# Performance work log

Hardware: AMD Instinct MI355X
Metric: run time of the kernel (lower is better)

Reference implementation:

```python
import jax, jax.numpy as jnp
import numpy as np

B, S, T = 4096, 32, 32   # batch (flattened words), source chars, target chars
V = 256                  # char vocab (source and target)
E, H, A = 128, 64, 64    # source embed, GRU units, attention dim
BOW = 1                  # begin-of-word token id


def setup_inputs() -> dict:
    key = jax.random.key(0)
    ks = iter(jax.random.split(key, 32))
    p = lambda shape: jax.random.normal(next(ks), shape, dtype=jnp.float32) * 0.05
    return {
        "src_ids": jax.random.randint(next(ks), (B, S), 0, V, dtype=jnp.int64),
        "tgt_ids": jax.random.randint(next(ks), (B, T), 0, V, dtype=jnp.int64),
        "src_emb": p((V, E)),
        "enc_Wf": p((E, 3 * H)), "enc_Uf": p((H, 3 * H)), "enc_bf": p((2, 3 * H)),
        "enc_Wb": p((E, 3 * H)), "enc_Ub": p((H, 3 * H)), "enc_bb": p((2, 3 * H)),
        "attn_We": p((H, A)), "attn_be": p((A,)),
        "attn_Wd": p((H, A)), "attn_bd": p((A,)),
        "attn_v": p((A, 1)), "attn_bv": p((1,)),
        "dec_W": p((H + H, 3 * H)), "dec_U": p((H, 3 * H)), "dec_b": p((2, 3 * H)),
        "out_W": p((H, V)), "out_b": p((V,)),
    }


def _gru_cell(h, x, W, U, b):
    # TF GRUCell with reset_after=True (default): separate input/recurrent biases
    xp = x @ W + b[0]
    hp = h @ U + b[1]
    xz, xr, xh = jnp.split(xp, 3, axis=-1)
    hz, hr, hh = jnp.split(hp, 3, axis=-1)
    z = jax.nn.sigmoid(xz + hz)
    r = jax.nn.sigmoid(xr + hr)
    n = jnp.tanh(xh + r * hh)
    return z * h + (1.0 - z) * n


def _gru_scan(xs, h0, W, U, b):
    # xs: [S, B, D] -> outputs [S, B, H]
    def step(h, x):
        h_new = _gru_cell(h, x, W, U, b)
        return h_new, h_new
    _, ys = jax.lax.scan(step, h0, xs)
    return ys


def reference(src_ids, tgt_ids, src_emb,
              enc_Wf, enc_Uf, enc_bf, enc_Wb, enc_Ub, enc_bb,
              attn_We, attn_be, attn_Wd, attn_bd, attn_v, attn_bv,
              dec_W, dec_U, dec_b, out_W, out_b):
    batch = src_ids.shape[0]
    # --- encoder: embedding + bidirectional GRU (merge_mode='sum') ---
    emb = src_emb[src_ids]                       # [B,S,E]
    xs = jnp.swapaxes(emb, 0, 1)                 # [S,B,E]
    h0 = jnp.zeros((batch, H), emb.dtype)
    fwd = _gru_scan(xs, h0, enc_Wf, enc_Uf, enc_bf)
    bwd = _gru_scan(xs[::-1], h0, enc_Wb, enc_Ub, enc_bb)[::-1]
    encoded = jnp.swapaxes(fwd + bwd, 0, 1)      # [B,S,H]

    # --- attention memory setup ---
    enc_proj = encoded @ attn_We + attn_be       # [B,S,A]

    # --- decoder inputs: BOW-prefixed teacher-forced targets, tied embedding ---
    dec_in = jnp.concatenate(
        [jnp.full((batch, 1), BOW, dtype=tgt_ids.dtype), tgt_ids[:, :-1]], axis=1)
    tied_table = out_W.T * jnp.sqrt(jnp.asarray(H, encoded.dtype))  # [V,H]
    dec_emb = tied_table[dec_in]                 # [B,T,H]

    # --- decoder: Bahdanau-attention GRU, scan over time ---
    def step(h, x):
        dproj = h @ attn_Wd + attn_bd                        # [B,A]
        s = jnp.tanh(dproj[:, None, :] + enc_proj)           # [B,S,A]
        logit = (s @ attn_v)[..., 0] + attn_bv[0]            # [B,S]
        w = jax.nn.softmax(logit, axis=1)                    # softmax over S
        ctx = jnp.einsum('bs,bsh->bh', w, encoded)           # [B,H]
        att_in = jnp.concatenate([x, ctx], axis=1)           # [B,2H]
        h_new = _gru_cell(h, att_in, dec_W, dec_U, dec_b)
        return h_new, h_new

    _, hs = jax.lax.scan(step, encoded[:, 0], jnp.swapaxes(dec_emb, 0, 1))
    hidden = jnp.swapaxes(hs, 0, 1)              # [B,T,H]
    logits = hidden @ out_W + out_b              # [B,T,V]
    return logits
```

## Files before the change

### kernel.cpp

```cpp
#include <hip/hip_runtime.h>
#include <hip/hip_bf16.h>

typedef unsigned short u16;
typedef __bf16  bf16x8 __attribute__((ext_vector_type(8)));
typedef float   f32x4  __attribute__((ext_vector_type(4)));
typedef unsigned int   u32x4 __attribute__((ext_vector_type(4)));
typedef unsigned short u16x4 __attribute__((ext_vector_type(4)));

union FragU { bf16x8 v; u16 u[8]; u32x4 q; };

__device__ __forceinline__ float b2f(u16 u) {
    unsigned int x = ((unsigned int)u) << 16;
    return __builtin_bit_cast(float, x);
}
__device__ __forceinline__ u16 f2b(float f) {
    unsigned int x = __builtin_bit_cast(unsigned int, f);
    unsigned int r = (x + 0x7fffu + ((x >> 16) & 1u)) >> 16;
    return (u16)r;
}
__device__ __forceinline__ float rcp_(float x) { return __builtin_amdgcn_rcpf(x); }
__device__ __forceinline__ float sigm_(float x) { return rcp_(1.0f + __expf(-x)); }
__device__ __forceinline__ float tanh_(float x) {
    float e = __expf(2.0f * x);
    return 1.0f - 2.0f * rcp_(e + 1.0f);
}
__device__ __forceinline__ bf16x8 load_afrag(const u16* s) {
    FragU f; f.q = *(const u32x4*)s; return f.v;
}
__device__ __forceinline__ f32x4 mfma16(bf16x8 a, bf16x8 b, f32x4 c) {
    return __builtin_amdgcn_mfma_f32_16x16x32_bf16(a, b, c, 0, 0, 0);
}
__device__ __forceinline__ void split2(float f, u16& hi, u16& lo) {
    hi = f2b(f); lo = f2b(f - b2f(hi));
}

template<int MODE, int K, int N>
__device__ __forceinline__ void gemm_body(
    const float* __restrict__ srcf, const u16* __restrict__ sh,
    const u16* __restrict__ sl, const u16* __restrict__ sh2,
    const u16* __restrict__ sl2, const float* __restrict__ W,
    const float* __restrict__ bias, float* __restrict__ outf,
    u16* __restrict__ outh, int rbase)
{
    constexpr int KP = K + 8;
    constexpr int LK = (K == 128) ? 7 : 6;
    __shared__ __attribute__((aligned(16))) u16 Ash[64 * KP];
    __shared__ __attribute__((aligned(16))) u16 Asl[64 * KP];

    const int tid  = threadIdx.x;
    const int lane = tid & 63, w = tid >> 6;
    const int q = lane >> 4, ln = lane & 15;

    for (int i = tid; i < 64 * K; i += 256) {
        int r = i >> LK, c = i & (K - 1);
        int rg = rbase + r;
        float f;
        if constexpr (MODE == 0)      f = srcf[rg * K + c];
        else if constexpr (MODE == 1) f = srcf[c * 256 + rg] * 8.0f;
        else if constexpr (MODE == 2)
            f = b2f(sh[rg * 64 + c]) + b2f(sl[rg * 64 + c])
              + b2f(sh2[rg * 64 + c]) + b2f(sl2[rg * 64 + c]);
        else                          f = b2f(sh[rg * 64 + c]) + b2f(sl[rg * 64 + c]);
        u16 hi, lo; split2(f, hi, lo);
        Ash[r * KP + c] = hi; Asl[r * KP + c] = lo;
    }

    constexpr int NT  = N / 64;
    constexpr int NKF = K / 32;
    FragU bfh[NT][NKF], bfl[NT][NKF];
    float bv[NT];
    const int cw = w * (N >> 2);
#pragma unroll
    for (int tl = 0; tl < NT; ++tl) {
        int col = cw + tl * 16 + ln;
#pragma unroll
        for (int kf = 0; kf < NKF; ++kf)
#pragma unroll
            for (int j = 0; j < 8; ++j) {
                float f = W[(kf * 32 + q * 8 + j) * N + col];
                split2(f, bfh[tl][kf].u[j], bfl[tl][kf].u[j]);
            }
        bv[tl] = bias[col];
    }
    __syncthreads();

#pragma unroll
    for (int r = 0; r < 4; ++r) {
        bf16x8 afh[NKF], afl[NKF];
#pragma unroll
        for (int kf = 0; kf < NKF; ++kf) {
            afh[kf] = load_afrag(&Ash[(r * 16 + ln) * KP + kf * 32 + q * 8]);
            afl[kf] = load_afrag(&Asl[(r * 16 + ln) * KP + kf * 32 + q * 8]);
        }
#pragma unroll
        for (int tl = 0; tl < NT; ++tl) {
            f32x4 acc = {0.f, 0.f, 0.f, 0.f};
#pragma unroll
            for (int kf = 0; kf < NKF; ++kf) {
                acc = mfma16(afl[kf], bfh[tl][kf].v, acc);
                acc = mfma16(afh[kf], bfl[tl][kf].v, acc);
                acc = mfma16(afh[kf], bfh[tl][kf].v, acc);
            }
            const int col = cw + tl * 16 + ln;
#pragma unroll
            for (int i = 0; i < 4; ++i) {
                int rowg = rbase + r * 16 + q * 4 + i;
                float val = acc[i] + bv[tl];
                if constexpr (MODE == 2) {
                    outh[rowg * 64 + col] = f2b(val * 2.0f);
                } else if constexpr (MODE == 3) {
                    outf[rowg * N + col] = val;
                } else {
                    outf[rowg * 192 + col] = val;
                }
            }
        }
    }
}

template<int MODE, int K, int N>
__global__ __launch_bounds__(256, (MODE >= 2) ? 2 : 1) void gemm_hl(
    const float* __restrict__ srcf, const u16* __restrict__ sh,
    const u16* __restrict__ sl, const u16* __restrict__ sh2,
    const u16* __restrict__ sl2, const float* __restrict__ W,
    const float* __restrict__ bias, float* __restrict__ outf,
    u16* __restrict__ outh)
{
    gemm_body<MODE, K, N>(srcf, sh, sl, sh2, sl2, W, bias, outf, outh,
                          (int)blockIdx.x * 64);
}

__global__ __launch_bounds__(256, 1) void xpv_all(
    const float* __restrict__ src_emb,
    const float* __restrict__ Wf, const float* __restrict__ bf, float* __restrict__ xf,
    const float* __restrict__ Wb, const float* __restrict__ bb, float* __restrict__ xb,
    const float* __restrict__ outW, const float* __restrict__ dW,
    const float* __restrict__ db, float* __restrict__ xd)
{
    const int b = blockIdx.x;
    if (b < 4)
        gemm_body<0, 128, 192>(src_emb, nullptr, nullptr, nullptr, nullptr,
                               Wf, bf, xf, nullptr, b * 64);
    else if (b < 8)
        gemm_body<0, 128, 192>(src_emb, nullptr, nullptr, nullptr, nullptr,
                               Wb, bb, xb, nullptr, (b - 4) * 64);
    else
        gemm_body<1, 64, 192>(outW, nullptr, nullptr, nullptr, nullptr,
                              dW, db, xd, nullptr, (b - 8) * 64);
}

__global__ __launch_bounds__(256, 2) void enc8(
    const int* __restrict__ src_ids, const float* __restrict__ xf,
    const float* __restrict__ xb,
    const float* __restrict__ Uf_, const float* __restrict__ bf_,
    const float* __restrict__ Ub_, const float* __restrict__ bb_,
    u16* __restrict__ fh, u16* __restrict__ fl,
    u16* __restrict__ bh, u16* __restrict__ bl)
{
    __shared__ __attribute__((aligned(16))) u16 hsh[16 * 72];
    __shared__ __attribute__((aligned(16))) u16 hsl[16 * 72];
    const int tid  = threadIdx.x;
    const int lane = tid & 63, w = tid >> 6;
    const int q = lane >> 4, ln = lane & 15;
    const int dir = (int)(blockIdx.x >> 9);
    const int b0  = (int)(blockIdx.x & 511) * 8;
    const float* xpv = dir ? xb  : xf;
    const float* U   = dir ? Ub_ : Uf_;
    const float* b_  = dir ? bb_ : bf_;
    u16* oh = dir ? bh : fh;
    u16* ol = dir ? bl : fl;
    const int jw = w * 16;
    const bool rowok = (q < 2);

    for (int i = tid; i < 16 * 64; i += 256) {
        int r = i >> 6, c = i & 63;
        hsh[r * 72 + c] = 0; hsl[r * 72 + c] = 0;
    }
    FragU ufh[3][2], ufl[3][2];
    float b1[3];
#pragma unroll
    for (int g = 0; g < 3; ++g) {
        int col = g * 64 + jw + ln;
#pragma unroll
        for (int kf = 0; kf < 2; ++kf)
#pragma unroll
            for (int j = 0; j < 8; ++j) {
                float f = U[(kf * 32 + q * 8 + j) * 192 + col];
                split2(f, ufh[g][kf].u[j], ufl[g][kf].u[j]);
            }
        b1[g] = b_[192 + col];
    }
    float hp[4] = {0, 0, 0, 0};

    float xg[3][4];
    {
        const int s0 = dir ? 31 : 0;
#pragma unroll
        for (int i = 0; i < 4; ++i) {
            int rowv = b0 + ((q * 4 + i) & 7);
            int id = src_ids[rowv * 32 + s0];
#pragma unroll
            for (int g = 0; g < 3; ++g) xg[g][i] = xpv[id * 192 + g * 64 + jw + ln];
        }
    }
    __syncthreads();

    for (int step = 0; step < 32; ++step) {
        const int s = dir ? (31 - step) : step;
        float xgn[3][4];
        {
            int sn = dir ? (step >= 31 ? 0 : 30 - step) : (step >= 31 ? 31 : step + 1);
#pragma unroll
            for (int i = 0; i < 4; ++i) {
                int rowv = b0 + ((q * 4 + i) & 7);
                int id = src_ids[rowv * 32 + sn];
#pragma unroll
                for (int g = 0; g < 3; ++g) xgn[g][i] = xpv[id * 192 + g * 64 + jw + ln];
            }
        }
        bf16x8 a0h = load_afrag(&hsh[ln * 72 + q * 8]);
        bf16x8 a1h = load_afrag(&hsh[ln * 72 + 32 + q * 8]);
        bf16x8 a0l = load_afrag(&hsl[ln * 72 + q * 8]);
        bf16x8 a1l = load_afrag(&hsl[ln * 72 + 32 + q * 8]);
        f32x4 acc[3];
#pragma unroll
        for (int g = 0; g < 3; ++g) {
            f32x4 a = {0.f, 0.f, 0.f, 0.f};
            a = mfma16(a0l, ufh[g][0].v, a);
            a = mfma16(a0h, ufl[g][0].v, a);
            a = mfma16(a0h, ufh[g][0].v, a);
            a = mfma16(a1l, ufh[g][1].v, a);
            a = mfma16(a1h, ufl[g][1].v, a);
            a = mfma16(a1h, ufh[g][1].v, a);
            acc[g] = a;
        }
        float nh[4];
#pragma unroll
        for (int i = 0; i < 4; ++i) {
            const int rowg = b0 + q * 4 + i;
            float zz = sigm_(xg[0][i] + acc[0][i] + b1[0]);
            float rr = sigm_(xg[1][i] + acc[1][i] + b1[1]);
            float nn = tanh_(xg[2][i] + rr * (acc[2][i] + b1[2]));
            nh[i] = zz * hp[i] + (1.0f - zz) * nn;  hp[i] = nh[i];
            if (rowok) {
                const int gidx = (rowg * 32 + s) * 64 + jw + ln;
                u16 hi, lo; split2(nh[i], hi, lo);
                oh[gidx] = hi; ol[gidx] = lo;
            }
        }
        __syncthreads();
        if (rowok) {
#pragma unroll
            for (int i = 0; i < 4; ++i) {
                u16 hi, lo; split2(nh[i], hi, lo);
                hsh[(q * 4 + i) * 72 + jw + ln] = hi;
                hsl[(q * 4 + i) * 72 + jw + ln] = lo;
            }
        }
        __syncthreads();
#pragma unroll
        for (int g = 0; g < 3; ++g)
#pragma unroll
            for (int i = 0; i < 4; ++i) xg[g][i] = xgn[g][i];
    }
}

__global__ __launch_bounds__(256, 2) void dec_kernel(
    const int* __restrict__ tgt_ids, const float* __restrict__ xpvd,
    const u16* __restrict__ fh, const u16* __restrict__ fl,
    const u16* __restrict__ bh, const u16* __restrict__ bl,
    const u16* __restrict__ encpT,
    const float* __restrict__ dec_U, const float* __restrict__ dec_W,
    const float* __restrict__ dec_b,
    const float* __restrict__ Wd, const float* __restrict__ bd,
    const float* __restrict__ v_, const float* __restrict__ bv_,
    u16* __restrict__ hid_hi, u16* __restrict__ hid_lo)
{
    __shared__ __attribute__((aligned(16))) float enc_lds[8 * 2048];
    __shared__ __attribute__((aligned(16))) u16 hqh[16 * 72];
    __shared__ __attribute__((aligned(16))) u16 hql[16 * 72];
    __shared__ __attribute__((aligned(16))) u16 cxh[16 * 72];
    __shared__ __attribute__((aligned(16))) u16 cxl[16 * 72];
    __shared__ __attribute__((aligned(16))) float dpl[8 * 72];
    __shared__ float wl[8 * 36];
    __shared__ float vl[64];
    const int tid  = threadIdx.x;
    const int lane = tid & 63, w = tid >> 6;
    const int q = lane >> 4, ln = lane & 15;
    const int b0 = blockIdx.x * 8;
    const int jw = w * 16;
    const bool rowok = (q < 2);

    {
        const u16* g0 = fh + (size_t)b0 * 2048;
        const u16* g1 = fl + (size_t)b0 * 2048;
        const u16* g2 = bh + (size_t)b0 * 2048;
        const u16* g3 = bl + (size_t)b0 * 2048;
        for (int i = tid; i < 8 * 2048 / 4; i += 256) {
            u16x4 v0 = *(const u16x4*)(g0 + i * 4);
            u16x4 v1 = *(const u16x4*)(g1 + i * 4);
            u16x4 v2 = *(const u16x4*)(g2 + i * 4);
            u16x4 v3 = *(const u16x4*)(g3 + i * 4);
            f32x4 f;
#pragma unroll
            for (int k = 0; k < 4; ++k)
                f[k] = (b2f(v0[k]) + b2f(v1[k])) + (b2f(v2[k]) + b2f(v3[k]));
            *(f32x4*)(&enc_lds[i * 4]) = f;
        }
    }
    if (tid < 64) vl[tid] = v_[tid];
    const float bv0 = bv_[0];

    FragU wdh[2], wdl[2], ufh[3][2], ufl[3][2], wch[3][2], wcl[3][2];
    float b1[3];
#pragma unroll
    for (int kf = 0; kf < 2; ++kf)
#pragma unroll
        for (int j = 0; j < 8; ++j) {
            float f = Wd[(kf * 32 + q * 8 + j) * 64 + jw + ln];
            split2(f, wdh[kf].u[j], wdl[kf].u[j]);
        }
#pragma unroll
    for (int g = 0; g < 3; ++g) {
        int col = g * 64 + jw + ln;
#pragma unroll
        for (int kf = 0; kf < 2; ++kf)
#pragma unroll
            for (int j = 0; j < 8; ++j) {
                int k = kf * 32 + q * 8 + j;
                float fu = dec_U[k * 192 + col];
                split2(fu, ufh[g][kf].u[j], ufl[g][kf].u[j]);
                float fc = dec_W[(64 + k) * 192 + col];
                split2(fc, wch[g][kf].u[j], wcl[g][kf].u[j]);
            }
        b1[g] = dec_b[192 + col];
    }
    const float bd_ = bd[jw + ln];

    const int bb2 = tid >> 5, ss = tid & 31;
    const u16* ep = &encpT[((size_t)(b0 + bb2) * 32 + ss) * 64];

    float xg[3][4];
#pragma unroll
    for (int g = 0; g < 3; ++g) {
        float f = xpvd[1 * 192 + g * 64 + jw + ln];
#pragma unroll
        for (int i = 0; i < 4; ++i) xg[g][i] = f;
    }
    __syncthreads();

    float SVB = bv0;
#pragma unroll
    for (int a = 0; a < 64; ++a) SVB += vl[a];

    for (int i = tid; i < 16 * 64; i += 256) {
        int r = i >> 6, c = i & 63;
        if (r < 8) {
            u16 hi, lo; split2(enc_lds[r * 2048 + c], hi, lo);
            hqh[r * 72 + c] = hi; hql[r * 72 + c] = lo;
        } else {
            hqh[r * 72 + c] = 0; hql[r * 72 + c] = 0;
            cxh[r * 72 + c] = 0; cxl[r * 72 + c] = 0;
        }
    }
    float hp[4];
#pragma unroll
    for (int i = 0; i < 4; ++i)
        hp[i] = rowok ? enc_lds[(q * 4 + i) * 2048 + jw + ln] : 0.f;
    __syncthreads();

    for (int t = 0; t < 32; ++t) {
        float xgn[3][4];
        {
            int tn = (t >= 31) ? 30 : t;
#pragma unroll
            for (int i = 0; i < 4; ++i) {
                int rowv = b0 + ((q * 4 + i) & 7);
                int id = tgt_ids[rowv * 32 + tn];
#pragma unroll
                for (int g = 0; g < 3; ++g) xgn[g][i] = xpvd[id * 192 + g * 64 + jw + ln];
            }
        }
        bf16x8 ah0 = load_afrag(&hqh[ln * 72 + q * 8]);
        bf16x8 ah1 = load_afrag(&hqh[ln * 72 + 32 + q * 8]);
        bf16x8 al0 = load_afrag(&hql[ln * 72 + q * 8]);
        bf16x8 al1 = load_afrag(&hql[ln * 72 + 32 + q * 8]);
        {
            f32x4 a = {0.f, 0.f, 0.f, 0.f};
            a = mfma16(al0, wdh[0].v, a);
            a = mfma16(ah0, wdl[0].v, a);
            a = mfma16(ah0, wdh[0].v, a);
            a = mfma16(al1, wdh[1].v, a);
            a = mfma16(ah1, wdl[1].v, a);
            a = mfma16(ah1, wdh[1].v, a);
            if (rowok) {
#pragma unroll
                for (int i = 0; i < 4; ++i)
                    dpl[(q * 4 + i) * 72 + jw + ln] = (a[i] + bd_) * 2.0f;
            }
        }
        __syncthreads();
        {
            const float* dp = &dpl[bb2 * 72];
            float av0 = 0.f, av1 = 0.f, av2 = 0.f, av3 = 0.f;
#pragma unroll
            for (int a8 = 0; a8 < 8; ++a8) {
                FragU ev; ev.q = *(const u32x4*)(ep + a8 * 8);
                f32x4 d0 = *(const f32x4*)(dp + a8 * 8);
                f32x4 d1 = *(const f32x4*)(dp + a8 * 8 + 4);
#pragma unroll
                for (int j = 0; j < 8; ++j) {
                    const int a = a8 * 8 + j;
                    float u = (j < 4 ? d0[j & 3] : d1[j & 3]) + b2f(ev.u[j]);
                    float E = __expf(u);
                    float rc = vl[a] * rcp_(E + 1.0f);
                    if ((j & 3) == 0)      av0 += rc;
                    else if ((j & 3) == 1) av1 += rc;
                    else if ((j & 3) == 2) av2 += rc;
                    else                   av3 += rc;
                }
            }
            float logit = SVB - 2.0f * ((av0 + av1) + (av2 + av3));
            float m = logit;
#pragma unroll
            for (int off = 16; off > 0; off >>= 1) m = fmaxf(m, __shfl_xor(m, off, 32));
            float e2 = __expf(logit - m);
            float ssum = e2;
#pragma unroll
            for (int off = 16; off > 0; off >>= 1) ssum += __shfl_xor(ssum, off, 32);
            wl[bb2 * 36 + ss] = e2 * rcp_(ssum);
        }
        __syncthreads();
#pragma unroll
        for (int rr2 = 0; rr2 < 2; ++rr2) {
            const int b = rr2 * 4 + w;
            float c0 = 0.f, c1 = 0.f, c2 = 0.f, c3 = 0.f;
#pragma unroll
            for (int s4 = 0; s4 < 8; ++s4) {
                const int s = s4 * 4 + q;
                const float ww = wl[b * 36 + s];
                f32x4 ev = *(const f32x4*)(&enc_lds[b * 2048 + s * 64 + ln * 4]);
                c0 += ww * ev[0]; c1 += ww * ev[1];
                c2 += ww * ev[2]; c3 += ww * ev[3];
            }
            c0 += __shfl_xor(c0, 16); c0 += __shfl_xor(c0, 32);
            c1 += __shfl_xor(c1, 16); c1 += __shfl_xor(c1, 32);
            c2 += __shfl_xor(c2, 16); c2 += __shfl_xor(c2, 32);
            c3 += __shfl_xor(c3, 16); c3 += __shfl_xor(c3, 32);
            if (q == 0) {
                u16x4 vh, vo;
                u16 th, tl2;
                split2(c0, th, tl2); vh[0] = th; vo[0] = tl2;
                split2(c1, th, tl2); vh[1] = th; vo[1] = tl2;
                split2(c2, th, tl2); vh[2] = th; vo[2] = tl2;
                split2(c3, th, tl2); vh[3] = th; vo[3] = tl2;
                *(u16x4*)(&cxh[b * 72 + ln * 4]) = vh;
                *(u16x4*)(&cxl[b * 72 + ln * 4]) = vo;
            }
        }
        __syncthreads();
        bf16x8 ac0 = load_afrag(&cxh[ln * 72 + q * 8]);
        bf16x8 ac1 = load_afrag(&cxh[ln * 72 + 32 + q * 8]);
        bf16x8 al2 = load_afrag(&cxl[ln * 72 + q * 8]);
        bf16x8 al3 = load_afrag(&cxl[ln * 72 + 32 + q * 8]);
        f32x4 ax[3], ahh[3];
#pragma unroll
        for (int g = 0; g < 3; ++g) {
            f32x4 a = {0.f, 0.f, 0.f, 0.f};
            a = mfma16(al2, wch[g][0].v, a);
            a = mfma16(ac0, wcl[g][0].v, a);
            a = mfma16(ac0, wch[g][0].v, a);
            a = mfma16(al3, wch[g][1].v, a);
            a = mfma16(ac1, wcl[g][1].v, a);
            a = mfma16(ac1, wch[g][1].v, a);
            ax[g] = a;
            f32x4 h = {0.f, 0.f, 0.f, 0.f};
            h = mfma16(al0, ufh[g][0].v, h);
            h = mfma16(ah0, ufl[g][0].v, h);
            h = mfma16(ah0, ufh[g][0].v, h);
            h = mfma16(al1, ufh[g][1].v, h);
            h = mfma16(ah1, ufl[g][1].v, h);
            h = mfma16(ah1, ufh[g][1].v, h);
            ahh[g] = h;
        }
        float nh[4];
#pragma unroll
        for (int i = 0; i < 4; ++i) {
            int rowg = b0 + q * 4 + i;
            float zz = sigm_(xg[0][i] + ax[0][i] + ahh[0][i] + b1[0]);
            float rr = sigm_(xg[1][i] + ax[1][i] + ahh[1][i] + b1[1]);
            float nn = tanh_(xg[2][i] + ax[2][i] + rr * (ahh[2][i] + b1[2]));
            nh[i] = zz * hp[i] + (1.0f - zz) * nn;  hp[i] = nh[i];
            if (rowok) {
                int gidx = (rowg * 32 + t) * 64 + jw + ln;
                u16 hi, lo; split2(nh[i], hi, lo);
                hid_hi[gidx] = hi; hid_lo[gidx] = lo;
                hqh[(q * 4 + i) * 72 + jw + ln] = hi;
                hql[(q * 4 + i) * 72 + jw + ln] = lo;
            }
        }
        __syncthreads();
#pragma unroll
        for (int g = 0; g < 3; ++g)
#pragma unroll
            for (int i = 0; i < 4; ++i) xg[g][i] = xgn[g][i];
    }
}

extern "C" void kernel_launch(void* const* d_in, const int* in_sizes, int n_in,
                              void* d_out, int out_size, void* d_ws, size_t ws_size,
                              hipStream_t stream) {
    const int*   src_ids = (const int*)d_in[0];
    const int*   tgt_ids = (const int*)d_in[1];
    const float* src_emb = (const float*)d_in[2];
    const float* enc_Wf  = (const float*)d_in[3];
    const float* enc_Uf  = (const float*)d_in[4];
    const float* enc_bf  = (const float*)d_in[5];
    const float* enc_Wb  = (const float*)d_in[6];
    const float* enc_Ub  = (const float*)d_in[7];
    const float* enc_bb  = (const float*)d_in[8];
    const float* attn_We = (const float*)d_in[9];
    const float* attn_be = (const float*)d_in[10];
    const float* attn_Wd = (const float*)d_in[11];
    const float* attn_bd = (const float*)d_in[12];
    const float* attn_v  = (const float*)d_in[13];
    const float* attn_bv = (const float*)d_in[14];
    const float* dec_W   = (const float*)d_in[15];
    const float* dec_U   = (const float*)d_in[16];
    const float* dec_b   = (const float*)d_in[17];
    const float* out_W   = (const float*)d_in[18];
    const float* out_b   = (const float*)d_in[19];

    u16* ws = (u16*)d_ws;
    u16* fwd_hi = ws;
    u16* fwd_lo = ws +  8388608;
    u16* bwd_hi = ws + 16777216;
    u16* bwd_lo = ws + 25165824;
    u16* encpT  = ws + 33554432;
    float* xpv_f = (float*)(ws + 41943040);
    float* xpv_b = (float*)(ws + 42041344);
    float* xpvd  = (float*)(ws + 42139648);
    u16* hid_hi = fwd_hi;
    u16* hid_lo = fwd_lo;

    dim3 blk(256);
    xpv_all<<<12, blk, 0, stream>>>(src_emb, enc_Wf, enc_bf, xpv_f,
                                    enc_Wb, enc_bb, xpv_b,
                                    out_W, dec_W, dec_b, xpvd);
    enc8<<<1024, blk, 0, stream>>>(src_ids, xpv_f, xpv_b, enc_Uf, enc_bf,
                                   enc_Ub, enc_bb, fwd_hi, fwd_lo, bwd_hi, bwd_lo);
    gemm_hl<2, 64, 64><<<2048, blk, 0, stream>>>(
        nullptr, fwd_hi, fwd_lo, bwd_hi, bwd_lo, attn_We, attn_be, nullptr, encpT);
    dec_kernel<<<512, blk, 0, stream>>>(tgt_ids, xpvd, fwd_hi, fwd_lo,
                                        bwd_hi, bwd_lo, encpT,
                                        dec_U, dec_W, dec_b,
                                        attn_Wd, attn_bd, attn_v, attn_bv,
                                        hid_hi, hid_lo);
    gemm_hl<3, 64, 256><<<2048, blk, 0, stream>>>(
        nullptr, hid_hi, hid_lo, nullptr, nullptr, out_W, out_b, (float*)d_out, nullptr);
}
```

Baseline: 693.0 us.

## Stream pre-split decoder weight fragments from global memory instead of holding them in registers

An extra block in the prep kernel now splits attn_Wd, dec_U and the context part of dec_W into bf16 hi/lo MFMA fragments and writes them to workspace. The decoder reloads these fragments from global (L2-resident) memory every timestep, using an opaque zero offset so they are not hoisted back into registers. This removes roughly a hundred VGPRs of persistent weight fragments to relieve register pressure and spilling. It also folds the z/r recurrent MFMAs into the input accumulator and drops the next-step prefetch of the target projection. The cost is extra per-step global/L2 traffic and load latency on the sequential critical path.

```diff
diff --git a/kernel.cpp b/kernel.cpp
--- a/kernel.cpp
+++ b/kernel.cpp
@@ -135,7 +135,9 @@
     const float* __restrict__ Wf, const float* __restrict__ bf, float* __restrict__ xf,
     const float* __restrict__ Wb, const float* __restrict__ bb, float* __restrict__ xb,
     const float* __restrict__ outW, const float* __restrict__ dW,
-    const float* __restrict__ db, float* __restrict__ xd)
+    const float* __restrict__ db, float* __restrict__ xd,
+    const float* __restrict__ dU, const float* __restrict__ Wd_,
+    u16* __restrict__ wf)
 {
     const int b = blockIdx.x;
     if (b < 4)
@@ -144,9 +146,38 @@
     else if (b < 8)
         gemm_body<0, 128, 192>(src_emb, nullptr, nullptr, nullptr, nullptr,
                                Wb, bb, xb, nullptr, (b - 4) * 64);
-    else
+    else if (b < 12)
         gemm_body<1, 64, 192>(outW, nullptr, nullptr, nullptr, nullptr,
                               dW, db, xd, nullptr, (b - 8) * 64);
+    else {
+        const int t2 = threadIdx.x;
+        const int lane = t2 & 63, w2 = t2 >> 6;
+        const int q = lane >> 4, ln = lane & 15;
+        const int jw = w2 * 16;
+#pragma unroll
+        for (int kf = 0; kf < 2; ++kf)
+#pragma unroll
+            for (int j = 0; j < 8; ++j) {
+                float f = Wd_[(kf * 32 + q * 8 + j) * 64 + jw + ln];
+                u16 hi, lo; split2(f, hi, lo);
+                wf[(t2 * 2 + kf) * 8 + j] = hi;
+                wf[4096 + (t2 * 2 + kf) * 8 + j] = lo;
+            }
+#pragma unroll
+        for (int g = 0; g < 3; ++g)
+#pragma unroll
+            for (int kf = 0; kf < 2; ++kf)
+#pragma unroll
+                for (int j = 0; j < 8; ++j) {
+                    int k = kf * 32 + q * 8 + j, col = g * 64 + jw + ln;
+                    int fi = ((t2 * 3 + g) * 2 + kf) * 8 + j;
+                    u16 hi, lo;
+                    split2(dU[k * 192 + col], hi, lo);
+                    wf[8192 + fi] = hi;  wf[20480 + fi] = lo;
+                    split2(dW[(64 + k) * 192 + col], hi, lo);
+                    wf[32768 + fi] = hi; wf[45056 + fi] = lo;
+                }
+    }
 }
 
 __global__ __launch_bounds__(256, 2) void enc8(
@@ -269,10 +300,8 @@
     const int* __restrict__ tgt_ids, const float* __restrict__ xpvd,
     const u16* __restrict__ fh, const u16* __restrict__ fl,
     const u16* __restrict__ bh, const u16* __restrict__ bl,
-    const u16* __restrict__ encpT,
-    const float* __restrict__ dec_U, const float* __restrict__ dec_W,
-    const float* __restrict__ dec_b,
-    const float* __restrict__ Wd, const float* __restrict__ bd,
+    const u16* __restrict__ encpT, const u16* __restrict__ wf,
+    const float* __restrict__ dec_b, const float* __restrict__ bd,
     const float* __restrict__ v_, const float* __restrict__ bv_,
     u16* __restrict__ hid_hi, u16* __restrict__ hid_lo)
 {
@@ -311,42 +340,14 @@
     if (tid < 64) vl[tid] = v_[tid];
     const float bv0 = bv_[0];
 
-    FragU wdh[2], wdl[2], ufh[3][2], ufl[3][2], wch[3][2], wcl[3][2];
     float b1[3];
 #pragma unroll
-    for (int kf = 0; kf < 2; ++kf)
-#pragma unroll
-        for (int j = 0; j < 8; ++j) {
-            float f = Wd[(kf * 32 + q * 8 + j) * 64 + jw + ln];
-            split2(f, wdh[kf].u[j], wdl[kf].u[j]);
-        }
-#pragma unroll
-    for (int g = 0; g < 3; ++g) {
-        int col = g * 64 + jw + ln;
-#pragma unroll
-        for (int kf = 0; kf < 2; ++kf)
-#pragma unroll
-            for (int j = 0; j < 8; ++j) {
-                int k = kf * 32 + q * 8 + j;
-                float fu = dec_U[k * 192 + col];
-                split2(fu, ufh[g][kf].u[j], ufl[g][kf].u[j]);
-                float fc = dec_W[(64 + k) * 192 + col];
-                split2(fc, wch[g][kf].u[j], wcl[g][kf].u[j]);
-            }
-        b1[g] = dec_b[192 + col];
-    }
+    for (int g = 0; g < 3; ++g) b1[g] = dec_b[192 + g * 64 + jw + ln];
     const float bd_ = bd[jw + ln];
 
     const int bb2 = tid >> 5, ss = tid & 31;
     const u16* ep = &encpT[((size_t)(b0 + bb2) * 32 + ss) * 64];
 
-    float xg[3][4];
-#pragma unroll
-    for (int g = 0; g < 3; ++g) {
-        float f = xpvd[1 * 192 + g * 64 + jw + ln];
-#pragma unroll
-        for (int i = 0; i < 4; ++i) xg[g][i] = f;
-    }
     __syncthreads();
 
     float SVB = bv0;
@@ -370,29 +371,36 @@
     __syncthreads();
 
     for (int t = 0; t < 32; ++t) {
-        float xgn[3][4];
-        {
-            int tn = (t >= 31) ? 30 : t;
-#pragma unroll
-            for (int i = 0; i < 4; ++i) {
-                int rowv = b0 + ((q * 4 + i) & 7);
-                int id = tgt_ids[rowv * 32 + tn];
-#pragma unroll
-                for (int g = 0; g < 3; ++g) xgn[g][i] = xpvd[id * 192 + g * 64 + jw + ln];
-            }
-        }
+        int zz = 0;
+        asm volatile("" : "+v"(zz));
+        const u16* wfp = wf + zz;
+
+        float xg[3][4];
+#pragma unroll
+        for (int i = 0; i < 4; ++i) {
+            int rowv = b0 + ((q * 4 + i) & 7);
+            int id = (t == 0) ? 1 : tgt_ids[rowv * 32 + (t - 1)];
+#pragma unroll
+            for (int g = 0; g < 3; ++g) xg[g][i] = xpvd[id * 192 + g * 64 + jw + ln];
+        }
+
         bf16x8 ah0 = load_afrag(&hqh[ln * 72 + q * 8]);
         bf16x8 ah1 = load_afrag(&hqh[ln * 72 + 32 + q * 8]);
         bf16x8 al0 = load_afrag(&hql[ln * 72 + q * 8]);
         bf16x8 al1 = load_afrag(&hql[ln * 72 + 32 + q * 8]);
         {
+            FragU d0h, d1h, d0l, d1l;
+            const u16* ph = wfp + (tid * 2) * 8;
+            const u16* pl = wfp + 4096 + (tid * 2) * 8;
+            d0h.q = *(const u32x4*)(ph);     d1h.q = *(const u32x4*)(ph + 8);
+            d0l.q = *(const u32x4*)(pl);     d1l.q = *(const u32x4*)(pl + 8);
             f32x4 a = {0.f, 0.f, 0.f, 0.f};
-            a = mfma16(al0, wdh[0].v, a);
-            a = mfma16(ah0, wdl[0].v, a);
-            a = mfma16(ah0, wdh[0].v, a);
-            a = mfma16(al1, wdh[1].v, a);
-            a = mfma16(ah1, wdl[1].v, a);
-            a = mfma16(ah1, wdh[1].v, a);
+            a = mfma16(al0, d0h.v, a);
+            a = mfma16(ah0, d0l.v, a);
+            a = mfma16(ah0, d0h.v, a);
+            a = mfma16(al1, d1h.v, a);
+            a = mfma16(ah1, d1l.v, a);
+            a = mfma16(ah1, d1h.v, a);
             if (rowok) {
 #pragma unroll
                 for (int i = 0; i < 4; ++i)
@@ -463,34 +471,54 @@
         bf16x8 ac1 = load_afrag(&cxh[ln * 72 + 32 + q * 8]);
         bf16x8 al2 = load_afrag(&cxl[ln * 72 + q * 8]);
         bf16x8 al3 = load_afrag(&cxl[ln * 72 + 32 + q * 8]);
-        f32x4 ax[3], ahh[3];
+        f32x4 zacc, racc, axn, ahn;
 #pragma unroll
         for (int g = 0; g < 3; ++g) {
+            FragU u0h, u1h, u0l, u1l, c0h, c1h, c0l, c1l;
+            const int fi = ((tid * 3 + g) * 2) * 8;
+            const u16* uph = wfp + 8192  + fi;
+            const u16* upl = wfp + 20480 + fi;
+            const u16* cph = wfp + 32768 + fi;
+            const u16* cpl = wfp + 45056 + fi;
+            u0h.q = *(const u32x4*)(uph); u1h.q = *(const u32x4*)(uph + 8);
+            u0l.q = *(const u32x4*)(upl); u1l.q = *(const u32x4*)(upl + 8);
+            c0h.q = *(const u32x4*)(cph); c1h.q = *(const u32x4*)(cph + 8);
+            c0l.q = *(const u32x4*)(cpl); c1l.q = *(const u32x4*)(cpl + 8);
             f32x4 a = {0.f, 0.f, 0.f, 0.f};
-            a = mfma16(al2, wch[g][0].v, a);
-            a = mfma16(ac0, wcl[g][0].v, a);
-            a = mfma16(ac0, wch[g][0].v, a);
-            a = mfma16(al3, wch[g][1].v, a);
-            a = mfma16(ac1, wcl[g][1].v, a);
-            a = mfma16(ac1, wch[g][1].v, a);
-            ax[g] = a;
-            f32x4 h = {0.f, 0.f, 0.f, 0.f};
-            h = mfma16(al0, ufh[g][0].v, h);
-            h = mfma16(ah0, ufl[g][0].v, h);
-            h = mfma16(ah0, ufh[g][0].v, h);
-            h = mfma16(al1, ufh[g][1].v, h);
-            h = mfma16(ah1, ufl[g][1].v, h);
-            h = mfma16(ah1, ufh[g][1].v, h);
-            ahh[g] = h;
+            a = mfma16(al2, c0h.v, a);
+            a = mfma16(ac0, c0l.v, a);
+            a = mfma16(ac0, c0h.v, a);
+            a = mfma16(al3, c1h.v, a);
+            a = mfma16(ac1, c1l.v, a);
+            a = mfma16(ac1, c1h.v, a);
+            if (g < 2) {
+                a = mfma16(al0, u0h.v, a);
+                a = mfma16(ah0, u0l.v, a);
+                a = mfma16(ah0, u0h.v, a);
+                a = mfma16(al1, u1h.v, a);
+                a = mfma16(ah1, u1l.v, a);
+                a = mfma16(ah1, u1h.v, a);
+                if (g == 0) zacc = a; else racc = a;
+            } else {
+                axn = a;
+                f32x4 h = {0.f, 0.f, 0.f, 0.f};
+                h = mfma16(al0, u0h.v, h);
+                h = mfma16(ah0, u0l.v, h);
+                h = mfma16(ah0, u0h.v, h);
+                h = mfma16(al1, u1h.v, h);
+                h = mfma16(ah1, u1l.v, h);
+                h = mfma16(ah1, u1h.v, h);
+                ahn = h;
+            }
         }
         float nh[4];
 #pragma unroll
         for (int i = 0; i < 4; ++i) {
             int rowg = b0 + q * 4 + i;
-            float zz = sigm_(xg[0][i] + ax[0][i] + ahh[0][i] + b1[0]);
-            float rr = sigm_(xg[1][i] + ax[1][i] + ahh[1][i] + b1[1]);
-            float nn = tanh_(xg[2][i] + ax[2][i] + rr * (ahh[2][i] + b1[2]));
-            nh[i] = zz * hp[i] + (1.0f - zz) * nn;  hp[i] = nh[i];
+            float zv = sigm_(xg[0][i] + zacc[i] + b1[0]);
+            float rv = sigm_(xg[1][i] + racc[i] + b1[1]);
+            float nn = tanh_(xg[2][i] + axn[i] + rv * (ahn[i] + b1[2]));
+            nh[i] = zv * hp[i] + (1.0f - zv) * nn;  hp[i] = nh[i];
             if (rowok) {
                 int gidx = (rowg * 32 + t) * 64 + jw + ln;
                 u16 hi, lo; split2(nh[i], hi, lo);
@@ -500,10 +528,6 @@
             }
         }
         __syncthreads();
-#pragma unroll
-        for (int g = 0; g < 3; ++g)
-#pragma unroll
-            for (int i = 0; i < 4; ++i) xg[g][i] = xgn[g][i];
     }
 }
 
@@ -540,21 +564,22 @@
     float* xpv_f = (float*)(ws + 41943040);
     float* xpv_b = (float*)(ws + 42041344);
     float* xpvd  = (float*)(ws + 42139648);
+    u16* wf      = ws + 42237952;
     u16* hid_hi = fwd_hi;
     u16* hid_lo = fwd_lo;
 
     dim3 blk(256);
-    xpv_all<<<12, blk, 0, stream>>>(src_emb, enc_Wf, enc_bf, xpv_f,
+    xpv_all<<<13, blk, 0, stream>>>(src_emb, enc_Wf, enc_bf, xpv_f,
                                     enc_Wb, enc_bb, xpv_b,
-                                    out_W, dec_W, dec_b, xpvd);
+                                    out_W, dec_W, dec_b, xpvd,
+                                    dec_U, attn_Wd, wf);
     enc8<<<1024, blk, 0, stream>>>(src_ids, xpv_f, xpv_b, enc_Uf, enc_bf,
                                    enc_Ub, enc_bb, fwd_hi, fwd_lo, bwd_hi, bwd_lo);
     gemm_hl<2, 64, 64><<<2048, blk, 0, stream>>>(
         nullptr, fwd_hi, fwd_lo, bwd_hi, bwd_lo, attn_We, attn_be, nullptr, encpT);
     dec_kernel<<<512, blk, 0, stream>>>(tgt_ids, xpvd, fwd_hi, fwd_lo,
-                                        bwd_hi, bwd_lo, encpT,
-                                        dec_U, dec_W, dec_b,
-                                        attn_Wd, attn_bd, attn_v, attn_bv,
+                                        bwd_hi, bwd_lo, encpT, wf,
+                                        dec_b, attn_bd, attn_v, attn_bv,
                                         hid_hi, hid_lo);
     gemm_hl<3, 64, 256><<<2048, blk, 0, stream>>>(
         nullptr, hid_hi, hid_lo, nullptr, nullptr, out_W, out_b, (float*)d_out, nullptr);
```

Measured after the change: 604.3 us. 1.15x faster.
